# Optimization experiments

Measured on AMD Instinct MI355X. Metric: run time of the kernel, lower is better.

The kernel has to match this reference:

```python
import jax, jax.numpy as jnp
import numpy as np

B, H, S, D = 2, 16, 2048, 128  # batch, heads, seq_len, head_dim (hidden=2048, heads=16)


def setup_inputs() -> dict:
    key = jax.random.key(0)
    kq, kk, kv = jax.random.split(key, 3)
    q = jax.random.normal(kq, (B, H, S, D), dtype=jnp.float32)
    k = jax.random.normal(kk, (B, H, S, D), dtype=jnp.float32)
    v = jax.random.normal(kv, (B, H, S, D), dtype=jnp.float32)
    return {"q": q, "k": k, "v": v}


def reference(q, k, v):
    # scores = (q @ k^T) / sqrt(head_dim)  -> [B, H, S, S]
    scaling = 1.0 / jnp.sqrt(jnp.asarray(q.shape[-1], dtype=q.dtype))
    scores = jnp.einsum('bhqd,bhkd->bhqk', q, k) * scaling
    # softmax over keys (dropout p=0.0 -> identity in eval / p=0)
    weights = jax.nn.softmax(scores, axis=-1)
    # out = weights @ v -> [B, H, S, D]
    return jnp.einsum('bhqk,bhkd->bhqd', weights, v)
```

## Files before the change

### kernel.cpp

```cpp
#include <hip/hip_runtime.h>
#include <stdint.h>

typedef __attribute__((ext_vector_type(4))) float f32x4;
typedef __attribute__((ext_vector_type(8))) short bf16x8;
typedef __attribute__((ext_vector_type(4))) short bf16x4;

constexpr int S_ = 2048;
constexpr int D_ = 128;
constexpr int BH = 32;
constexpr int KB = 64;
constexpr int NT = S_ / KB;
constexpr float QSCALE = 0.08838834764831845f * 1.4426950408889634f;

__device__ __forceinline__ short f2bf(float f) {
  uint32_t u = __float_as_uint(f);
  u += 0x7fffu + ((u >> 16) & 1u);
  return (short)(u >> 16);
}
__device__ __forceinline__ short f2bf_fast(float f) {
  return (short)((__float_as_uint(f) + 0x8000u) >> 16);
}

__device__ __forceinline__ void gll16(const void* g, void* l) {
  __builtin_amdgcn_global_load_lds(
      (const __attribute__((address_space(1))) void*)g,
      (__attribute__((address_space(3))) void*)l, 16, 0, 0);
}

__global__ void prep_k(const float* __restrict__ k, short* __restrict__ kb) {
  const size_t N8 = (size_t)BH * S_ * D_ / 8;
  size_t i = (size_t)blockIdx.x * blockDim.x + threadIdx.x;
  const size_t stride = (size_t)gridDim.x * blockDim.x;
  for (; i < N8; i += stride) {
    float4 a = reinterpret_cast<const float4*>(k)[i * 2];
    float4 b = reinterpret_cast<const float4*>(k)[i * 2 + 1];
    bf16x8 o;
    o[0] = f2bf(a.x); o[1] = f2bf(a.y); o[2] = f2bf(a.z); o[3] = f2bf(a.w);
    o[4] = f2bf(b.x); o[5] = f2bf(b.y); o[6] = f2bf(b.z); o[7] = f2bf(b.w);
    reinterpret_cast<bf16x8*>(kb)[i] = o;
  }
}

__global__ void prep_vt(const float* __restrict__ v, short* __restrict__ vt) {
  __shared__ __align__(16) short Lt[64][136];
  const int bh = blockIdx.x >> 5;
  const int s0 = (blockIdx.x & 31) * 64;
  const int t = threadIdx.x;
#pragma unroll
  for (int i = 0; i < 4; ++i) {
    int g = t + 256 * i;
    int r = g >> 4, c8 = g & 15;
    const float* src = v + ((size_t)bh * S_ + s0 + r) * D_ + c8 * 8;
    float4 f0 = *reinterpret_cast<const float4*>(src);
    float4 f1 = *reinterpret_cast<const float4*>(src + 4);
    bf16x8 o;
    o[0] = f2bf(f0.x); o[1] = f2bf(f0.y); o[2] = f2bf(f0.z); o[3] = f2bf(f0.w);
    o[4] = f2bf(f1.x); o[5] = f2bf(f1.y); o[6] = f2bf(f1.z); o[7] = f2bf(f1.w);
    *reinterpret_cast<bf16x8*>(&Lt[r][c8 * 8]) = o;
  }
  __syncthreads();
#pragma unroll
  for (int i = 0; i < 4; ++i) {
    int g = t * 4 + i;
    int d = g >> 3, s8 = g & 7;
    bf16x8 o;
#pragma unroll
    for (int j = 0; j < 8; ++j) o[j] = Lt[s8 * 8 + j][d];
    *reinterpret_cast<bf16x8*>(&vt[((size_t)bh * D_ + d) * S_ + s0 + s8 * 8]) = o;
  }
}

__global__ __launch_bounds__(256, 2) void attn_fwd_v3(
    const float* __restrict__ q, const short* __restrict__ kbf,
    const short* __restrict__ vt, float* __restrict__ out)
{
  __shared__ __align__(16) short Klds[2][64 * 128];
  __shared__ __align__(16) short Vlds[2][128 * 64];
  __shared__ __align__(16) short Plds[4][32 * 64];

  const int lid = blockIdx.x;
  const int swz = (lid & 7) * 64 + (lid >> 3);
  const int qt = swz & 15;
  const int bh = swz >> 4;

  const int tid = threadIdx.x;
  const int wid = tid >> 6;
  const int lane = tid & 63;
  const int l16 = lane & 15;
  const int lhi = lane >> 4;

  const int qrow0 = qt * 128 + wid * 32;

  bf16x8 aq[2][4];
#pragma unroll
  for (int qs = 0; qs < 2; ++qs)
#pragma unroll
    for (int ks = 0; ks < 4; ++ks) {
      const float* p = q + ((size_t)bh * S_ + qrow0 + qs * 16 + l16) * D_ + ks * 32 + lhi * 8;
      float4 f0 = *reinterpret_cast<const float4*>(p);
      float4 f1 = *reinterpret_cast<const float4*>(p + 4);
      bf16x8 a;
      a[0] = f2bf(f0.x * QSCALE); a[1] = f2bf(f0.y * QSCALE);
      a[2] = f2bf(f0.z * QSCALE); a[3] = f2bf(f0.w * QSCALE);
      a[4] = f2bf(f1.x * QSCALE); a[5] = f2bf(f1.y * QSCALE);
      a[6] = f2bf(f1.z * QSCALE); a[7] = f2bf(f1.w * QSCALE);
      aq[qs][ks] = a;
    }

  const short* kg = kbf + (size_t)bh * S_ * D_;
  const short* vg = vt + (size_t)bh * D_ * S_;

  int koff[4], voff[4];
#pragma unroll
  for (int j = 0; j < 4; ++j) {
    const int krow = wid * 16 + j * 4 + lhi;
    koff[j] = krow * D_ + ((l16 ^ (krow & 7)) * 8);
    const int vd = wid * 32 + j * 8 + (lane >> 3);
    voff[j] = vd * S_ + (((lane & 7) ^ (vd & 7)) * 8);
  }

  auto stage = [&](int buf, int kv0) {
    const short* ksrc = kg + (size_t)kv0 * D_;
    const short* vsrc = vg + kv0;
#pragma unroll
    for (int j = 0; j < 4; ++j)
      gll16(ksrc + koff[j], &Klds[buf][wid * 2048 + j * 512]);
#pragma unroll
    for (int j = 0; j < 4; ++j)
      gll16(vsrc + voff[j], &Vlds[buf][wid * 2048 + j * 512]);
  };

  float m[2] = {-1e30f, -1e30f}, l[2] = {0.f, 0.f};
  f32x4 oacc[2][8];
#pragma unroll
  for (int qs = 0; qs < 2; ++qs)
#pragma unroll
    for (int i = 0; i < 8; ++i) oacc[qs][i] = (f32x4){0.f, 0.f, 0.f, 0.f};

  short* Pw = &Plds[wid][0];

  stage(0, 0);
  int cur = 0;
  for (int t = 0; t < NT; ++t) {
    __syncthreads();
    if (t + 1 < NT) stage(cur ^ 1, (t + 1) * KB);

    f32x4 sf[2][4];
#pragma unroll
    for (int qs = 0; qs < 2; ++qs)
#pragma unroll
      for (int kbb = 0; kbb < 4; ++kbb) sf[qs][kbb] = (f32x4){0.f, 0.f, 0.f, 0.f};
    __builtin_amdgcn_s_setprio(1);
#pragma unroll
    for (int kbb = 0; kbb < 4; ++kbb) {
      const int rowk = kbb * 16 + l16;
#pragma unroll
      for (int ks = 0; ks < 4; ++ks) {
        bf16x8 ak = *reinterpret_cast<const bf16x8*>(
            &Klds[cur][rowk * D_ + (((ks * 4 + lhi) ^ (rowk & 7)) * 8)]);
        sf[0][kbb] = __builtin_amdgcn_mfma_f32_16x16x32_bf16(ak, aq[0][ks], sf[0][kbb], 0, 0, 0);
        sf[1][kbb] = __builtin_amdgcn_mfma_f32_16x16x32_bf16(ak, aq[1][ks], sf[1][kbb], 0, 0, 0);
      }
    }
    __builtin_amdgcn_s_setprio(0);

#pragma unroll
    for (int qs = 0; qs < 2; ++qs) {
      float pm = fmaxf(fmaxf(fmaxf(sf[qs][0][0], sf[qs][0][1]), fmaxf(sf[qs][0][2], sf[qs][0][3])),
                       fmaxf(fmaxf(sf[qs][1][0], sf[qs][1][1]), fmaxf(sf[qs][1][2], sf[qs][1][3])));
      pm = fmaxf(pm, fmaxf(fmaxf(fmaxf(sf[qs][2][0], sf[qs][2][1]), fmaxf(sf[qs][2][2], sf[qs][2][3])),
                           fmaxf(fmaxf(sf[qs][3][0], sf[qs][3][1]), fmaxf(sf[qs][3][2], sf[qs][3][3]))));
      pm = fmaxf(pm, __shfl_xor(pm, 16, 64));
      pm = fmaxf(pm, __shfl_xor(pm, 32, 64));
      if (__any(pm > m[qs] + 8.f)) {
        const float mo = m[qs];
        const float mn = fmaxf(mo, pm);
        m[qs] = mn;
        const float al = exp2f(mo - mn);
        l[qs] *= al;
#pragma unroll
        for (int d0 = 0; d0 < 8; ++d0) oacc[qs][d0] *= al;
      }
      const int qrow = qs * 16 + l16;
      float ps = 0.f;
#pragma unroll
      for (int kbb = 0; kbb < 4; ++kbb) {
        bf16x4 pw;
#pragma unroll
        for (int r = 0; r < 4; ++r) {
          float p = exp2f(sf[qs][kbb][r] - m[qs]);
          ps += p;
          pw[r] = f2bf_fast(p);
        }
        *reinterpret_cast<bf16x4*>(
            &Pw[qrow * 64 + (((2 * kbb + (lhi >> 1)) ^ (qrow & 7)) * 8) + ((lhi & 1) * 4)]) = pw;
      }
      ps += __shfl_xor(ps, 16, 64);
      ps += __shfl_xor(ps, 32, 64);
      l[qs] += ps;
    }

    __builtin_amdgcn_s_setprio(1);
#pragma unroll
    for (int kc = 0; kc < 2; ++kc) {
      bf16x8 pb[2];
#pragma unroll
      for (int qs = 0; qs < 2; ++qs) {
        const int qrow = qs * 16 + l16;
        pb[qs] = *reinterpret_cast<const bf16x8*>(
            &Pw[qrow * 64 + (((4 * kc + lhi) ^ (qrow & 7)) * 8)]);
      }
#pragma unroll
      for (int d0 = 0; d0 < 8; ++d0) {
        const int vd = d0 * 16 + l16;
        bf16x8 av = *reinterpret_cast<const bf16x8*>(
            &Vlds[cur][vd * 64 + (((4 * kc + lhi) ^ (vd & 7)) * 8)]);
        oacc[0][d0] = __builtin_amdgcn_mfma_f32_16x16x32_bf16(av, pb[0], oacc[0][d0], 0, 0, 0);
        oacc[1][d0] = __builtin_amdgcn_mfma_f32_16x16x32_bf16(av, pb[1], oacc[1][d0], 0, 0, 0);
      }
    }
    __builtin_amdgcn_s_setprio(0);
    cur ^= 1;
  }

#pragma unroll
  for (int qs = 0; qs < 2; ++qs) {
    const float inv = 1.0f / l[qs];
    float* ob = out + ((size_t)bh * S_ + qrow0 + qs * 16 + l16) * D_;
#pragma unroll
    for (int d0 = 0; d0 < 8; ++d0) {
      float4 o4 = {oacc[qs][d0][0] * inv, oacc[qs][d0][1] * inv,
                   oacc[qs][d0][2] * inv, oacc[qs][d0][3] * inv};
      *reinterpret_cast<float4*>(ob + d0 * 16 + lhi * 4) = o4;
    }
  }
}

__global__ __launch_bounds__(256, 4) void attn_fwd_v1(
    const float* __restrict__ q, const float* __restrict__ k,
    const float* __restrict__ v, float* __restrict__ out)
{
  __shared__ __align__(16) short Klds[32 * 128];
  __shared__ __align__(16) short Vlds[128 * 40];
  __shared__ __align__(16) short Plds[4][16 * 40];
  const int lid = blockIdx.x;
  const int swz = (lid & 7) * 128 + (lid >> 3);
  const int qt = swz & 31;
  const int bh = swz >> 5;
  const int tid = threadIdx.x;
  const int wid = tid >> 6;
  const int lane = tid & 63;
  const int l16 = lane & 15;
  const int lhi = lane >> 4;
  const int qrow0 = qt * 64 + wid * 16;
  const float* qg = q + ((size_t)bh * S_ + qrow0 + l16) * D_;
  const float* kg = k + (size_t)bh * S_ * D_;
  const float* vg = v + (size_t)bh * S_ * D_;
  bf16x8 aq[4];
#pragma unroll
  for (int ks = 0; ks < 4; ++ks) {
    const float* p = qg + ks * 32 + lhi * 8;
    float4 f0 = *reinterpret_cast<const float4*>(p);
    float4 f1 = *reinterpret_cast<const float4*>(p + 4);
    bf16x8 a;
    a[0] = f2bf(f0.x * QSCALE); a[1] = f2bf(f0.y * QSCALE);
    a[2] = f2bf(f0.z * QSCALE); a[3] = f2bf(f0.w * QSCALE);
    a[4] = f2bf(f1.x * QSCALE); a[5] = f2bf(f1.y * QSCALE);
    a[6] = f2bf(f1.z * QSCALE); a[7] = f2bf(f1.w * QSCALE);
    aq[ks] = a;
  }
  float mrow[4], lrow[4];
  f32x4 oacc[8];
#pragma unroll
  for (int r = 0; r < 4; ++r) { mrow[r] = -1e30f; lrow[r] = 0.f; }
#pragma unroll
  for (int i = 0; i < 8; ++i) oacc[i] = (f32x4){0.f, 0.f, 0.f, 0.f};
  for (int t = 0; t < S_ / 32; ++t) {
    const int kv0 = t * 32;
    __syncthreads();
#pragma unroll
    for (int i = 0; i < 2; ++i) {
      const int g = tid * 2 + i;
      const int row = g >> 4;
      const int c8 = g & 15;
      const float* ksrc = kg + (size_t)(kv0 + row) * D_ + c8 * 8;
      float4 f0 = *reinterpret_cast<const float4*>(ksrc);
      float4 f1 = *reinterpret_cast<const float4*>(ksrc + 4);
      bf16x8 kk;
      kk[0] = f2bf(f0.x); kk[1] = f2bf(f0.y); kk[2] = f2bf(f0.z); kk[3] = f2bf(f0.w);
      kk[4] = f2bf(f1.x); kk[5] = f2bf(f1.y); kk[6] = f2bf(f1.z); kk[7] = f2bf(f1.w);
      *reinterpret_cast<bf16x8*>(
          &Klds[row * D_ + ((c8 * 8) ^ ((row & 7) << 3))]) = kk;
      const float* vsrc = vg + (size_t)(kv0 + row) * D_ + c8 * 8;
      float4 g0 = *reinterpret_cast<const float4*>(vsrc);
      float4 g1 = *reinterpret_cast<const float4*>(vsrc + 4);
      const int dbase = c8 * 8;
      Vlds[(dbase + 0) * 40 + row] = f2bf(g0.x);
      Vlds[(dbase + 1) * 40 + row] = f2bf(g0.y);
      Vlds[(dbase + 2) * 40 + row] = f2bf(g0.z);
      Vlds[(dbase + 3) * 40 + row] = f2bf(g0.w);
      Vlds[(dbase + 4) * 40 + row] = f2bf(g1.x);
      Vlds[(dbase + 5) * 40 + row] = f2bf(g1.y);
      Vlds[(dbase + 6) * 40 + row] = f2bf(g1.z);
      Vlds[(dbase + 7) * 40 + row] = f2bf(g1.w);
    }
    __syncthreads();
    f32x4 sfrag[2];
#pragma unroll
    for (int kb = 0; kb < 2; ++kb) {
      f32x4 acc = (f32x4){0.f, 0.f, 0.f, 0.f};
#pragma unroll
      for (int ks = 0; ks < 4; ++ks) {
        const int rowk = kb * 16 + l16;
        bf16x8 bk = *reinterpret_cast<const bf16x8*>(
            &Klds[rowk * D_ + (((ks * 4 + lhi) * 8) ^ ((rowk & 7) << 3))]);
        acc = __builtin_amdgcn_mfma_f32_16x16x32_bf16(aq[ks], bk, acc, 0, 0, 0);
      }
      sfrag[kb] = acc;
    }
    float mt[4];
#pragma unroll
    for (int r = 0; r < 4; ++r) mt[r] = fmaxf(sfrag[0][r], sfrag[1][r]);
#pragma unroll
    for (int off = 1; off < 16; off <<= 1)
#pragma unroll
      for (int r = 0; r < 4; ++r) mt[r] = fmaxf(mt[r], __shfl_xor(mt[r], off, 64));
    float al[4], ps[4];
#pragma unroll
    for (int r = 0; r < 4; ++r) {
      float mn = fmaxf(mrow[r], mt[r]);
      al[r] = exp2f(mrow[r] - mn);
      mrow[r] = mn;
      ps[r] = 0.f;
    }
#pragma unroll
    for (int kb = 0; kb < 2; ++kb)
#pragma unroll
      for (int r = 0; r < 4; ++r) {
        float p = exp2f(sfrag[kb][r] - mrow[r]);
        ps[r] += p;
        Plds[wid][(lhi * 4 + r) * 40 + kb * 16 + l16] = f2bf(p);
      }
#pragma unroll
    for (int off = 1; off < 16; off <<= 1)
#pragma unroll
      for (int r = 0; r < 4; ++r) ps[r] += __shfl_xor(ps[r], off, 64);
#pragma unroll
    for (int r = 0; r < 4; ++r) lrow[r] = lrow[r] * al[r] + ps[r];
#pragma unroll
    for (int i = 0; i < 8; ++i)
#pragma unroll
      for (int r = 0; r < 4; ++r) oacc[i][r] *= al[r];
    bf16x8 ap = *reinterpret_cast<const bf16x8*>(&Plds[wid][l16 * 40 + lhi * 8]);
#pragma unroll
    for (int d0 = 0; d0 < 8; ++d0) {
      bf16x8 bv = *reinterpret_cast<const bf16x8*>(
          &Vlds[(d0 * 16 + l16) * 40 + lhi * 8]);
      oacc[d0] = __builtin_amdgcn_mfma_f32_16x16x32_bf16(ap, bv, oacc[d0], 0, 0, 0);
    }
  }
#pragma unroll
  for (int r = 0; r < 4; ++r) {
    float inv = 1.0f / lrow[r];
    float* orow = out + ((size_t)bh * S_ + qrow0 + lhi * 4 + r) * D_ + l16;
#pragma unroll
    for (int d0 = 0; d0 < 8; ++d0) orow[d0 * 16] = oacc[d0][r] * inv;
  }
}

extern "C" void kernel_launch(void* const* d_in, const int* in_sizes, int n_in,
                              void* d_out, int out_size, void* d_ws, size_t ws_size,
                              hipStream_t stream) {
  (void)in_sizes; (void)n_in; (void)out_size;
  const float* q = (const float*)d_in[0];
  const float* k = (const float*)d_in[1];
  const float* v = (const float*)d_in[2];
  float* o = (float*)d_out;
  const size_t NEL = (size_t)BH * S_ * D_;
  const size_t need = NEL * 2 * sizeof(short);
  if (ws_size >= need) {
    short* kb = (short*)d_ws;
    short* vt = kb + NEL;
    hipLaunchKernelGGL(prep_k, dim3(2048), dim3(256), 0, stream, k, kb);
    hipLaunchKernelGGL(prep_vt, dim3(1024), dim3(256), 0, stream, v, vt);
    hipLaunchKernelGGL(attn_fwd_v3, dim3(512), dim3(256), 0, stream, q, kb, vt, o);
  } else {
    hipLaunchKernelGGL(attn_fwd_v1, dim3(1024), dim3(256), 0, stream, q, k, v, o);
  }
}
```

Baseline: 128.2 us.

## Switch attention to 32x32x16 MFMA with register-resident P via permlane32 swap

Rewrites the main attention kernel to use 32x32x16 bf16 MFMA tiles instead of 16x16x32. Each lane now owns one query row, which simplifies the row max and sum reductions. The probability matrix stays in registers: it is packed with v_cvt_pk_bf16_f32 and rearranged with v_permlane32_swap, so the LDS staging buffer and its round trip go away. K and V LDS layouts are changed to a fragment-ordered, unswizzled layout, which may cause LDS bank conflicts. The conversion of P to bf16 now uses round-to-nearest-even rather than the earlier cheap rounding.

After: 126.2 us. No clear change (-1.6%).

```diff
diff --git a/kernel.cpp b/kernel.cpp
--- a/kernel.cpp
+++ b/kernel.cpp
@@ -2,8 +2,8 @@
 #include <stdint.h>
 
 typedef __attribute__((ext_vector_type(4))) float f32x4;
+typedef __attribute__((ext_vector_type(16))) float f32x16;
 typedef __attribute__((ext_vector_type(8))) short bf16x8;
-typedef __attribute__((ext_vector_type(4))) short bf16x4;
 
 constexpr int S_ = 2048;
 constexpr int D_ = 128;
@@ -16,9 +16,6 @@
   uint32_t u = __float_as_uint(f);
   u += 0x7fffu + ((u >> 16) & 1u);
   return (short)(u >> 16);
-}
-__device__ __forceinline__ short f2bf_fast(float f) {
-  return (short)((__float_as_uint(f) + 0x8000u) >> 16);
 }
 
 __device__ __forceinline__ void gll16(const void* g, void* l) {
@@ -70,13 +67,12 @@
   }
 }
 
-__global__ __launch_bounds__(256, 2) void attn_fwd_v3(
+__global__ __launch_bounds__(256, 2) void attn_fwd_v4(
     const float* __restrict__ q, const short* __restrict__ kbf,
     const short* __restrict__ vt, float* __restrict__ out)
 {
   __shared__ __align__(16) short Klds[2][64 * 128];
   __shared__ __align__(16) short Vlds[2][128 * 64];
-  __shared__ __align__(16) short Plds[4][32 * 64];
 
   const int lid = blockIdx.x;
   const int swz = (lid & 7) * 64 + (lid >> 3);
@@ -86,58 +82,47 @@
   const int tid = threadIdx.x;
   const int wid = tid >> 6;
   const int lane = tid & 63;
-  const int l16 = lane & 15;
-  const int lhi = lane >> 4;
-
-  const int qrow0 = qt * 128 + wid * 32;
-
-  bf16x8 aq[2][4];
-#pragma unroll
-  for (int qs = 0; qs < 2; ++qs)
-#pragma unroll
-    for (int ks = 0; ks < 4; ++ks) {
-      const float* p = q + ((size_t)bh * S_ + qrow0 + qs * 16 + l16) * D_ + ks * 32 + lhi * 8;
-      float4 f0 = *reinterpret_cast<const float4*>(p);
-      float4 f1 = *reinterpret_cast<const float4*>(p + 4);
+  const int l32 = lane & 31;
+  const int hi = lane >> 5;
+
+  const int qrow = qt * 128 + wid * 32 + l32;
+
+  bf16x8 bq[8];
+  {
+    const float* qg = q + ((size_t)bh * S_ + qrow) * D_ + hi * 8;
+#pragma unroll
+    for (int s = 0; s < 8; ++s) {
+      float4 f0 = *reinterpret_cast<const float4*>(qg + s * 16);
+      float4 f1 = *reinterpret_cast<const float4*>(qg + s * 16 + 4);
       bf16x8 a;
       a[0] = f2bf(f0.x * QSCALE); a[1] = f2bf(f0.y * QSCALE);
       a[2] = f2bf(f0.z * QSCALE); a[3] = f2bf(f0.w * QSCALE);
       a[4] = f2bf(f1.x * QSCALE); a[5] = f2bf(f1.y * QSCALE);
       a[6] = f2bf(f1.z * QSCALE); a[7] = f2bf(f1.w * QSCALE);
-      aq[qs][ks] = a;
-    }
+      bq[s] = a;
+    }
+  }
 
   const short* kg = kbf + (size_t)bh * S_ * D_;
   const short* vg = vt + (size_t)bh * D_ * S_;
 
-  int koff[4], voff[4];
-#pragma unroll
-  for (int j = 0; j < 4; ++j) {
-    const int krow = wid * 16 + j * 4 + lhi;
-    koff[j] = krow * D_ + ((l16 ^ (krow & 7)) * 8);
-    const int vd = wid * 32 + j * 8 + (lane >> 3);
-    voff[j] = vd * S_ + (((lane & 7) ^ (vd & 7)) * 8);
-  }
-
   auto stage = [&](int buf, int kv0) {
-    const short* ksrc = kg + (size_t)kv0 * D_;
-    const short* vsrc = vg + kv0;
 #pragma unroll
     for (int j = 0; j < 4; ++j)
-      gll16(ksrc + koff[j], &Klds[buf][wid * 2048 + j * 512]);
+      gll16(kg + (size_t)kv0 * D_ + lane * D_ + (j * 4 + wid) * 8,
+            &Klds[buf][(j * 256 + wid * 64) * 8]);
 #pragma unroll
     for (int j = 0; j < 4; ++j)
-      gll16(vsrc + voff[j], &Vlds[buf][wid * 2048 + j * 512]);
+      gll16(vg + kv0 + (size_t)((wid & 1) * 64 + lane) * S_ + (j * 2 + (wid >> 1)) * 8,
+            &Vlds[buf][(j * 256 + wid * 64) * 8]);
   };
 
-  float m[2] = {-1e30f, -1e30f}, l[2] = {0.f, 0.f};
-  f32x4 oacc[2][8];
-#pragma unroll
-  for (int qs = 0; qs < 2; ++qs)
-#pragma unroll
-    for (int i = 0; i < 8; ++i) oacc[qs][i] = (f32x4){0.f, 0.f, 0.f, 0.f};
-
-  short* Pw = &Plds[wid][0];
+  float m = -1e30f, l = 0.f;
+  f32x16 oacc[4];
+#pragma unroll
+  for (int d0 = 0; d0 < 4; ++d0)
+#pragma unroll
+    for (int r = 0; r < 16; ++r) oacc[d0][r] = 0.f;
 
   stage(0, 0);
   int cur = 0;
@@ -145,95 +130,94 @@
     __syncthreads();
     if (t + 1 < NT) stage(cur ^ 1, (t + 1) * KB);
 
-    f32x4 sf[2][4];
-#pragma unroll
-    for (int qs = 0; qs < 2; ++qs)
-#pragma unroll
-      for (int kbb = 0; kbb < 4; ++kbb) sf[qs][kbb] = (f32x4){0.f, 0.f, 0.f, 0.f};
+    const short* Kb = &Klds[cur][0];
+    const short* Vb = &Vlds[cur][0];
+
+    f32x16 sf0, sf1;
+#pragma unroll
+    for (int r = 0; r < 16; ++r) { sf0[r] = 0.f; sf1[r] = 0.f; }
     __builtin_amdgcn_s_setprio(1);
 #pragma unroll
-    for (int kbb = 0; kbb < 4; ++kbb) {
-      const int rowk = kbb * 16 + l16;
-#pragma unroll
-      for (int ks = 0; ks < 4; ++ks) {
-        bf16x8 ak = *reinterpret_cast<const bf16x8*>(
-            &Klds[cur][rowk * D_ + (((ks * 4 + lhi) ^ (rowk & 7)) * 8)]);
-        sf[0][kbb] = __builtin_amdgcn_mfma_f32_16x16x32_bf16(ak, aq[0][ks], sf[0][kbb], 0, 0, 0);
-        sf[1][kbb] = __builtin_amdgcn_mfma_f32_16x16x32_bf16(ak, aq[1][ks], sf[1][kbb], 0, 0, 0);
-      }
+    for (int s = 0; s < 8; ++s) {
+      bf16x8 k0 = *reinterpret_cast<const bf16x8*>(
+          &Kb[((s * 2 + hi) * 64 + l32) * 8]);
+      bf16x8 k1 = *reinterpret_cast<const bf16x8*>(
+          &Kb[((s * 2 + hi) * 64 + 32 + l32) * 8]);
+      sf0 = __builtin_amdgcn_mfma_f32_32x32x16_bf16(k0, bq[s], sf0, 0, 0, 0);
+      sf1 = __builtin_amdgcn_mfma_f32_32x32x16_bf16(k1, bq[s], sf1, 0, 0, 0);
     }
     __builtin_amdgcn_s_setprio(0);
 
-#pragma unroll
-    for (int qs = 0; qs < 2; ++qs) {
-      float pm = fmaxf(fmaxf(fmaxf(sf[qs][0][0], sf[qs][0][1]), fmaxf(sf[qs][0][2], sf[qs][0][3])),
-                       fmaxf(fmaxf(sf[qs][1][0], sf[qs][1][1]), fmaxf(sf[qs][1][2], sf[qs][1][3])));
-      pm = fmaxf(pm, fmaxf(fmaxf(fmaxf(sf[qs][2][0], sf[qs][2][1]), fmaxf(sf[qs][2][2], sf[qs][2][3])),
-                           fmaxf(fmaxf(sf[qs][3][0], sf[qs][3][1]), fmaxf(sf[qs][3][2], sf[qs][3][3]))));
-      pm = fmaxf(pm, __shfl_xor(pm, 16, 64));
-      pm = fmaxf(pm, __shfl_xor(pm, 32, 64));
-      if (__any(pm > m[qs] + 8.f)) {
-        const float mo = m[qs];
-        const float mn = fmaxf(mo, pm);
-        m[qs] = mn;
-        const float al = exp2f(mo - mn);
-        l[qs] *= al;
-#pragma unroll
-        for (int d0 = 0; d0 < 8; ++d0) oacc[qs][d0] *= al;
-      }
-      const int qrow = qs * 16 + l16;
-      float ps = 0.f;
-#pragma unroll
-      for (int kbb = 0; kbb < 4; ++kbb) {
-        bf16x4 pw;
-#pragma unroll
-        for (int r = 0; r < 4; ++r) {
-          float p = exp2f(sf[qs][kbb][r] - m[qs]);
-          ps += p;
-          pw[r] = f2bf_fast(p);
-        }
-        *reinterpret_cast<bf16x4*>(
-            &Pw[qrow * 64 + (((2 * kbb + (lhi >> 1)) ^ (qrow & 7)) * 8) + ((lhi & 1) * 4)]) = pw;
-      }
-      ps += __shfl_xor(ps, 16, 64);
-      ps += __shfl_xor(ps, 32, 64);
-      l[qs] += ps;
-    }
-
-    __builtin_amdgcn_s_setprio(1);
-#pragma unroll
-    for (int kc = 0; kc < 2; ++kc) {
-      bf16x8 pb[2];
-#pragma unroll
-      for (int qs = 0; qs < 2; ++qs) {
-        const int qrow = qs * 16 + l16;
-        pb[qs] = *reinterpret_cast<const bf16x8*>(
-            &Pw[qrow * 64 + (((4 * kc + lhi) ^ (qrow & 7)) * 8)]);
-      }
-#pragma unroll
-      for (int d0 = 0; d0 < 8; ++d0) {
-        const int vd = d0 * 16 + l16;
-        bf16x8 av = *reinterpret_cast<const bf16x8*>(
-            &Vlds[cur][vd * 64 + (((4 * kc + lhi) ^ (vd & 7)) * 8)]);
-        oacc[0][d0] = __builtin_amdgcn_mfma_f32_16x16x32_bf16(av, pb[0], oacc[0][d0], 0, 0, 0);
-        oacc[1][d0] = __builtin_amdgcn_mfma_f32_16x16x32_bf16(av, pb[1], oacc[1][d0], 0, 0, 0);
-      }
-    }
-    __builtin_amdgcn_s_setprio(0);
+    float pm = fmaxf(sf0[0], sf0[1]);
+#pragma unroll
+    for (int r = 2; r < 16; ++r) pm = fmaxf(pm, sf0[r]);
+#pragma unroll
+    for (int r = 0; r < 16; ++r) pm = fmaxf(pm, sf1[r]);
+    pm = fmaxf(pm, __shfl_xor(pm, 32, 64));
+    if (__any(pm > m + 8.f)) {
+      const float mo = m;
+      m = fmaxf(mo, pm);
+      const float al = exp2f(mo - m);
+      l *= al;
+#pragma unroll
+      for (int d0 = 0; d0 < 4; ++d0)
+#pragma unroll
+        for (int r = 0; r < 16; ++r) oacc[d0][r] *= al;
+    }
+
+    float ps = 0.f;
+#define PROCESS_CHUNK(SF, C)                                                    \
+    {                                                                           \
+      uint32_t w[8];                                                            \
+      _Pragma("unroll")                                                         \
+      for (int i2 = 0; i2 < 8; ++i2) {                                          \
+        float e0 = exp2f(SF[2 * i2] - m);                                       \
+        float e1 = exp2f(SF[2 * i2 + 1] - m);                                   \
+        ps += e0 + e1;                                                          \
+        asm("v_cvt_pk_bf16_f32 %0, %1, %2" : "=v"(w[i2]) : "v"(e0), "v"(e1));   \
+      }                                                                         \
+      asm("v_permlane32_swap_b32 %0, %1" : "+v"(w[0]), "+v"(w[2]));             \
+      asm("v_permlane32_swap_b32 %0, %1" : "+v"(w[1]), "+v"(w[3]));             \
+      asm("v_permlane32_swap_b32 %0, %1" : "+v"(w[4]), "+v"(w[6]));             \
+      asm("v_permlane32_swap_b32 %0, %1" : "+v"(w[5]), "+v"(w[7]));             \
+      union { int4 i4; bf16x8 b; } u0, u1;                                      \
+      u0.i4 = (int4){(int)w[0], (int)w[1], (int)w[2], (int)w[3]};               \
+      u1.i4 = (int4){(int)w[4], (int)w[5], (int)w[6], (int)w[7]};               \
+      __builtin_amdgcn_s_setprio(1);                                            \
+      _Pragma("unroll")                                                         \
+      for (int d0 = 0; d0 < 4; ++d0) {                                          \
+        bf16x8 av = *reinterpret_cast<const bf16x8*>(                           \
+            &Vb[(((C) * 4 + hi) * 128 + d0 * 32 + l32) * 8]);                   \
+        oacc[d0] = __builtin_amdgcn_mfma_f32_32x32x16_bf16(av, u0.b, oacc[d0], 0, 0, 0); \
+      }                                                                         \
+      _Pragma("unroll")                                                         \
+      for (int d0 = 0; d0 < 4; ++d0) {                                          \
+        bf16x8 av = *reinterpret_cast<const bf16x8*>(                           \
+            &Vb[(((C) * 4 + 2 + hi) * 128 + d0 * 32 + l32) * 8]);               \
+        oacc[d0] = __builtin_amdgcn_mfma_f32_32x32x16_bf16(av, u1.b, oacc[d0], 0, 0, 0); \
+      }                                                                         \
+      __builtin_amdgcn_s_setprio(0);                                            \
+    }
+
+    PROCESS_CHUNK(sf0, 0)
+    PROCESS_CHUNK(sf1, 1)
+#undef PROCESS_CHUNK
+
+    ps += __shfl_xor(ps, 32, 64);
+    l += ps;
     cur ^= 1;
   }
 
-#pragma unroll
-  for (int qs = 0; qs < 2; ++qs) {
-    const float inv = 1.0f / l[qs];
-    float* ob = out + ((size_t)bh * S_ + qrow0 + qs * 16 + l16) * D_;
-#pragma unroll
-    for (int d0 = 0; d0 < 8; ++d0) {
-      float4 o4 = {oacc[qs][d0][0] * inv, oacc[qs][d0][1] * inv,
-                   oacc[qs][d0][2] * inv, oacc[qs][d0][3] * inv};
-      *reinterpret_cast<float4*>(ob + d0 * 16 + lhi * 4) = o4;
-    }
-  }
+  const float inv = 1.0f / l;
+  float* ob = out + ((size_t)bh * S_ + qrow) * D_;
+#pragma unroll
+  for (int d0 = 0; d0 < 4; ++d0)
+#pragma unroll
+    for (int r2 = 0; r2 < 4; ++r2) {
+      float4 o4 = {oacc[d0][r2 * 4 + 0] * inv, oacc[d0][r2 * 4 + 1] * inv,
+                   oacc[d0][r2 * 4 + 2] * inv, oacc[d0][r2 * 4 + 3] * inv};
+      *reinterpret_cast<float4*>(ob + d0 * 32 + r2 * 8 + hi * 4) = o4;
+    }
 }
 
 __global__ __launch_bounds__(256, 4) void attn_fwd_v1(
@@ -383,7 +367,7 @@
     short* vt = kb + NEL;
     hipLaunchKernelGGL(prep_k, dim3(2048), dim3(256), 0, stream, k, kb);
     hipLaunchKernelGGL(prep_vt, dim3(1024), dim3(256), 0, stream, v, vt);
-    hipLaunchKernelGGL(attn_fwd_v3, dim3(512), dim3(256), 0, stream, q, kb, vt, o);
+    hipLaunchKernelGGL(attn_fwd_v4, dim3(512), dim3(256), 0, stream, q, kb, vt, o);
   } else {
     hipLaunchKernelGGL(attn_fwd_v1, dim3(1024), dim3(256), 0, stream, q, k, v, o);
   }
```
